# Performance work log

Measured on AMD Instinct MI355X. Metric: run time of the kernel, lower is better.

## Reference

```python
import jax, jax.numpy as jnp
import numpy as np

NUM_CLASSES = 2
CONF_THRESH = 0.05
NMS_THRESH = 0.3
NMS_TOP_K = 5000
TOP_K = 750
VAR0, VAR1 = 0.1, 0.2
NEG = -1e9  # sentinel for suppressed / below-threshold scores

NUM = 16
PRIORS = 131072


def setup_inputs() -> dict:
    key = jax.random.key(0)
    k1, k2, k3 = jax.random.split(key, 3)
    loc_data = jax.random.normal(k1, (NUM, PRIORS, 4), dtype=jnp.float32)
    conf_data = jax.random.uniform(k2, (NUM * PRIORS, NUM_CLASSES), dtype=jnp.float32)
    prior_data = jax.random.uniform(k3, (PRIORS, 4), dtype=jnp.float32)
    return {"loc_data": loc_data, "conf_data": conf_data, "prior_data": prior_data}


def decode(loc, priors):
    # loc, priors: [N, 4] (cx, cy, w, h priors); SSD box decode -> (x1, y1, x2, y2)
    xy = priors[:, :2] + loc[:, :2] * VAR0 * priors[:, 2:]
    wh = priors[:, 2:] * jnp.exp(loc[:, 2:] * VAR1)
    return jnp.concatenate([xy - wh * 0.5, xy + wh * 0.5], axis=-1)


def _area(b):
    return (b[..., 2] - b[..., 0]) * (b[..., 3] - b[..., 1])


def iou_one_to_many(box, boxes):
    # box: [4], boxes: [K, 4]
    lt = jnp.maximum(box[:2], boxes[:, :2])
    rb = jnp.minimum(box[2:], boxes[:, 2:])
    wh = jnp.clip(rb - lt, 0.0)
    inter = wh[:, 0] * wh[:, 1]
    union = _area(box) + _area(boxes) - inter
    return inter / jnp.maximum(union, 1e-12)


def nms_single(boxes, scores):
    # boxes: [P, 4], scores: [P] (one image, one class) -> [TOP_K, 5] (score, x1, y1, x2, y2)
    s = jnp.where(scores > CONF_THRESH, scores, NEG)
    top_s, top_i = jax.lax.top_k(s, NMS_TOP_K)
    top_b = boxes[top_i]  # [K, 4]
    idx_range = jnp.arange(NMS_TOP_K)

    def step(s_work, _):
        idx = jnp.argmax(s_work)
        sc = s_work[idx]
        valid = sc > NEG * 0.5
        box = top_b[idx]
        ious = iou_one_to_many(box, top_b)
        kill = (ious > NMS_THRESH) | (idx_range == idx)
        s_new = jnp.where(kill, NEG, s_work)
        row = jnp.where(valid, jnp.concatenate([sc[None], box]), jnp.zeros((5,), boxes.dtype))
        return s_new, row

    _, rows = jax.lax.scan(step, top_s, None, length=TOP_K)
    return rows  # [TOP_K, 5]


def reference(loc_data, conf_data, prior_data):
    num, P, _ = loc_data.shape
    conf = conf_data.reshape(num, P, NUM_CLASSES).transpose(0, 2, 1)  # [num, C, P]
    batch_priors = jnp.broadcast_to(prior_data, (num, P, 4)).reshape(-1, 4)
    boxes = decode(loc_data.reshape(-1, 4), batch_priors).reshape(num, P, 4)
    # NMS over non-background classes, vmapped over batch and class
    per_image = jax.vmap(nms_single, in_axes=(None, 0))          # over classes
    det = jax.vmap(per_image)(boxes, conf[:, 1:, :])             # [num, C-1, TOP_K, 5]
    bg = jnp.zeros((num, 1, TOP_K, 5), det.dtype)
    return jnp.concatenate([bg, det], axis=1)                     # [num, C, TOP_K, 5]
```

## Files before the change

### kernel.cpp

```cpp
#include <hip/hip_runtime.h>
#include <cmath>

#pragma clang fp contract(off)

typedef unsigned long long ull;

#define NPRIORS 131072
#define NIMG 16
#define KSEL 5000
#define TOPK 750
#define SORTN 8192
#define MW 80
#define NCHUNK 79
#define KSELP (NCHUNK * 64)
#define NBIN 65536
#define NSLOT 16

#define MID03 0.30000002682209014892578125

#define WS_PAIRS 0
#define WS_NDIAG 0
#define WS_MCNT 1048576
#define WS_BOXES 1048832
#define WS_SCORES 2328832
#define WS_MASK 2649088
#define WS_HIST (WS_MASK)
#define WS_CNT  (WS_MASK + 4194304)
#define WS_POS  (WS_MASK + 8388608)
#define WS_DIAG (WS_MASK + (size_t)NIMG * KSEL * MW * 8)

__device__ inline ull readlane64(ull t, int l) {
  unsigned lo = (unsigned)__builtin_amdgcn_readlane((int)(unsigned)t, l);
  unsigned hi = (unsigned)__builtin_amdgcn_readlane((int)(unsigned)(t >> 32), l);
  return ((ull)hi << 32) | lo;
}

__global__ __launch_bounds__(256) void hist_kernel(const float* __restrict__ conf,
                                                   unsigned int* __restrict__ hist) {
  const int img = blockIdx.y;
  const float4* c4 = (const float4*)conf + (size_t)img * (NPRIORS / 2);
  unsigned int* H = hist + (size_t)img * NBIN;
  for (int q = blockIdx.x * 256 + threadIdx.x; q < NPRIORS / 2; q += 64 * 256) {
    float4 v = c4[q];
    if (v.y > 0.05f) atomicAdd(&H[(__float_as_uint(v.y) >> 12) & 0xFFFFu], 1u);
    if (v.w > 0.05f) atomicAdd(&H[(__float_as_uint(v.w) >> 12) & 0xFFFFu], 1u);
  }
}

__global__ __launch_bounds__(1024) void cutoff_kernel(const unsigned int* __restrict__ hist,
                                                      unsigned int* __restrict__ pos,
                                                      int* __restrict__ meta,
                                                      float4* __restrict__ sboxes,
                                                      float* __restrict__ sscores) {
  const int img = blockIdx.x;
  const int tid = threadIdx.x;
  const int lane = tid & 63;
  const int wv = tid >> 6;
  const unsigned int* H = hist + (size_t)img * NBIN;
  unsigned int* P = pos + (size_t)img * NBIN;
  __shared__ unsigned int csum[1024];
  __shared__ unsigned int suf[1024];
  __shared__ int s_cc;
  __shared__ unsigned int s_cut, s_mc;

  for (int g = 0; g < 64; ++g) {
    unsigned int v = H[g * 1024 + tid];
    for (int m = 1; m < 64; m <<= 1) v += __shfl_xor(v, m);
    if (lane == 0) csum[g * 16 + wv] = v;
  }
  __syncthreads();
  suf[tid] = csum[tid];
  if (tid == 0) s_cc = 0;
  __syncthreads();
  for (int off = 1; off < 1024; off <<= 1) {
    unsigned int v = (tid + off < 1024) ? suf[tid + off] : 0u;
    __syncthreads();
    suf[tid] += v;
    __syncthreads();
  }
  if (suf[tid] >= KSEL && (suf[tid] - csum[tid]) < KSEL) s_cc = tid;
  __syncthreads();
  const int cc = s_cc;
  if (tid == 0) { s_cut = (unsigned int)(cc * 64); s_mc = suf[0]; }
  __syncthreads();
  for (int b = cc * 64 + tid; b < NBIN; b += 1024) {
    int q = b >> 6;
    unsigned int acc = (q + 1 < 1024) ? suf[q + 1] : 0u;
    for (int b2 = b + 1; b2 < (q + 1) * 64; ++b2) acc += H[b2];
    P[b] = acc;
    unsigned int h = H[b];
    if (acc < KSEL && acc + h >= KSEL) { s_cut = (unsigned int)b; s_mc = acc + h; }
  }
  __syncthreads();
  if (tid == 0) {
    meta[img] = (int)min(s_mc, (unsigned int)SORTN);
    meta[16 + img] = (int)s_cut;
  }
  for (int i = tid; i < KSEL; i += 1024) {
    sboxes[(size_t)img * KSEL + i] = make_float4(0.f, 0.f, 0.f, 0.f);
    sscores[(size_t)img * KSEL + i] = -1e9f;
  }
}

__global__ __launch_bounds__(256) void scatter_kernel(const float* __restrict__ conf,
                                                      const unsigned int* __restrict__ pos,
                                                      unsigned int* __restrict__ cnt,
                                                      const int* __restrict__ meta,
                                                      ull* __restrict__ pairs) {
  const int img = blockIdx.y;
  const float4* c4 = (const float4*)conf + (size_t)img * (NPRIORS / 2);
  const unsigned int* P = pos + (size_t)img * NBIN;
  unsigned int* Cn = cnt + (size_t)img * NBIN;
  ull* mypairs = pairs + (size_t)img * SORTN;
  const unsigned int cutval = ((unsigned int)meta[16 + img]) << 12;
  for (int q = blockIdx.x * 256 + threadIdx.x; q < NPRIORS / 2; q += 64 * 256) {
    float4 v = c4[q];
#pragma unroll
    for (int h = 0; h < 2; ++h) {
      float sc = h ? v.w : v.y;
      unsigned int p = 2 * (unsigned int)q + h;
      if (sc > 0.05f) {
        unsigned int u = __float_as_uint(sc);
        if (u >= cutval) {
          unsigned int bin = (u >> 12) & 0xFFFFu;
          unsigned int slot = atomicAdd(&Cn[bin], 1u);
          unsigned int idx = P[bin] + slot;
          if (idx < SORTN)
            mypairs[idx] = ((ull)u << 32) | (ull)(0xFFFFFFFFu - p);
        }
      }
    }
  }
}

__global__ __launch_bounds__(256) void rank_decode_kernel(const ull* __restrict__ pairs,
                                                          const unsigned int* __restrict__ hist,
                                                          const unsigned int* __restrict__ pos,
                                                          const int* __restrict__ meta,
                                                          const float* __restrict__ loc,
                                                          const float* __restrict__ prior,
                                                          float4* __restrict__ sboxes,
                                                          float* __restrict__ sscores) {
#pragma clang fp contract(off)
  const int img = blockIdx.y;
  const int s = blockIdx.x * 256 + threadIdx.x;
  const int mc = meta[img];
  if (s >= mc) return;
  const ull* mypairs = pairs + (size_t)img * SORTN;
  const ull key = mypairs[s];
  const unsigned int u = (unsigned int)(key >> 32);
  const unsigned int bin = (u >> 12) & 0xFFFFu;
  const unsigned int base = pos[(size_t)img * NBIN + bin];
  const unsigned int cb = hist[(size_t)img * NBIN + bin];
  const int end = min((int)(base + cb), mc);
  int rank = 0;
  for (int j = (int)base; j < end; ++j) rank += (mypairs[j] > key);
  const int fp = (int)base + rank;
  if (fp >= KSEL) return;
  const unsigned int p = 0xFFFFFFFFu - (unsigned int)(key & 0xFFFFFFFFu);
  const float* lp = loc + ((size_t)img * NPRIORS + p) * 4;
  const float* pp = prior + (size_t)p * 4;
  float l0 = lp[0], l1 = lp[1], l2 = lp[2], l3 = lp[3];
  float px = pp[0], py = pp[1], pw = pp[2], ph = pp[3];
  float cx = px + (l0 * 0.1f) * pw;
  float cy = py + (l1 * 0.1f) * ph;
  float w = pw * (float)exp((double)(l2 * 0.2f));
  float hh = ph * (float)exp((double)(l3 * 0.2f));
  float4 box;
  box.x = cx - w * 0.5f;
  box.y = cy - hh * 0.5f;
  box.z = cx + w * 0.5f;
  box.w = cy + hh * 0.5f;
  sboxes[(size_t)img * KSEL + fp] = box;
  sscores[(size_t)img * KSEL + fp] = __uint_as_float(u);
}

__global__ __launch_bounds__(256) void mask_build_kernel(const float4* __restrict__ sboxes,
                                                         ull* __restrict__ mask,
                                                         ull* __restrict__ diag,
                                                         ull* __restrict__ ndiag) {
#pragma clang fp contract(off)
  const int jt = blockIdx.x;
  const int sp = blockIdx.y;
  const int img = blockIdx.z;
  if (jt < (sp >> 1)) return;
  const int tid = threadIdx.x;
  const int lane = tid & 63;
  const int wave = tid >> 6;
  __shared__ float4 ib[128];
  const float4* bb = sboxes + (size_t)img * KSEL;
  if (tid < 128) {
    int i = sp * 128 + tid;
    ib[tid] = (i < KSEL) ? bb[i] : make_float4(0.f, 0.f, 0.f, 0.f);
  }
  __syncthreads();
  float4 cb[4];
  float ca[4];
#pragma unroll
  for (int s = 0; s < 4; ++s) {
    int j = jt * 256 + s * 64 + lane;
    cb[s] = (j < KSEL) ? bb[j] : make_float4(0.f, 0.f, 0.f, 0.f);
    ca[s] = (cb[s].z - cb[s].x) * (cb[s].w - cb[s].y);
  }
  ull* mrow = mask + (size_t)img * KSEL * MW;
  ull* dg = diag + (size_t)img * KSELP;
  ull* ndg = ndiag + (size_t)img * KSELP;
  const int grp0 = jt * 4;
  for (int k = 0; k < 32; ++k) {
    const int rr = wave * 32 + k;
    const int strip = 2 * sp + (rr >> 6);
    const int r = rr & 63;
    const int i = sp * 128 + rr;
    const float4 pb = ib[rr];
    const float pa = (pb.z - pb.x) * (pb.w - pb.y);
    ull w[4];
#pragma unroll
    for (int s = 0; s < 4; ++s) {
      float ltx = fmaxf(pb.x, cb[s].x), lty = fmaxf(pb.y, cb[s].y);
      float rbx = fminf(pb.z, cb[s].z), rby = fminf(pb.w, cb[s].w);
      float ww = fmaxf(rbx - ltx, 0.0f), hh = fmaxf(rby - lty, 0.0f);
      float inter = ww * hh;
      float uni = fmaxf(pa + ca[s] - inter, 1e-12f);
      bool cond = ((grp0 + s) != strip) | (lane > r);
      bool kill = cond && ((double)inter > MID03 * (double)uni);
      w[s] = __ballot(kill);
    }
    if (lane == 0 && i < KSEL) {
      ull* wp = mrow + (size_t)i * MW + grp0;
      ((ulonglong2*)wp)[0] = make_ulonglong2(w[0], w[1]);
      ((ulonglong2*)wp)[1] = make_ulonglong2(w[2], w[3]);
#pragma unroll
      for (int s = 0; s < 4; ++s) {
        if (grp0 + s == strip) dg[i] = w[s];
        if (grp0 + s == strip + 1) ndg[i] = w[s];
      }
    }
  }
}

__global__ __launch_bounds__(64) void sweep_kernel(const ull* __restrict__ mask,
                                                   const ull* __restrict__ diag,
                                                   const ull* __restrict__ ndiag,
                                                   const float4* __restrict__ sboxes,
                                                   const float* __restrict__ sscores,
                                                   const int* __restrict__ meta,
                                                   float* __restrict__ out) {
  const int img = blockIdx.x;
  const int lane = threadIdx.x;
  const int V = min(meta[img], KSEL);
  const ull* mb = mask + (size_t)img * KSEL * MW;
  const ull* dg = diag + (size_t)img * KSELP;
  const ull* ng = ndiag + (size_t)img * KSELP;
  __shared__ ull stage[2 * NSLOT * 128];
  __shared__ int picks[TOPK];
  __shared__ int s_n;
  const int lc = min(lane, 39);

  ull rlo = 0ULL, rhi = 0ULL;
  int nkeep = 0;

  if (V > 0) {
    int reg = 0;
    bool pendingPrev = false;
    int lastrow = 0;
    ull bridge = 0ULL;
    ull dw = dg[lane];
    ull ndw = ng[lane];
    for (int c = 0; c * 64 < V; ++c) {
      const int base = c * 64;
      const int nidx = min(base + 64 + lane, KSELP - 1);
      ull dwn = dg[nidx];
      ull ndwn = ng[nidx];
      ull t = (c & 1) ? rhi : rlo;
      ull cur = readlane64(t, c >> 1) | bridge;
      bridge = 0ULL;
      const int lim = V - base;
      ull validm = (lim >= 64) ? ~0ULL : ((~0ULL) >> (64 - lim));
      ull avail = (~cur) & validm;

      int nb = 0;
      bool full = false;
      while (avail != 0ULL) {
        int r = __builtin_ctzll(avail);
        int row = base + r;
        if (lane == 0) picks[nkeep] = row;
        lastrow = row;
        nkeep++;
        if (nkeep >= TOPK) { full = true; break; }
        __builtin_amdgcn_global_load_lds(
            (const __attribute__((address_space(1))) unsigned int*)(mb + (size_t)row * MW + 2 * lc),
            (__attribute__((address_space(3))) unsigned int*)&stage[(reg * NSLOT + nb) * 128], 16, 0, 0);
        nb++;
        ull dr = readlane64(dw, r);
        bridge |= readlane64(ndw, r);
        avail &= ~(dr | (1ULL << r));
        if (nb == NSLOT) {
          if (pendingPrev) {
            __builtin_amdgcn_s_waitcnt(0x4F70);
            asm volatile("" ::: "memory");
#pragma unroll
            for (int q = 0; q < NSLOT; ++q) {
              ulonglong2 v = *(ulonglong2*)&stage[((1 - reg) * NSLOT + q) * 128 + 2 * lane];
              rlo |= v.x; rhi |= v.y;
            }
          }
          pendingPrev = true;
          reg = 1 - reg;
          nb = 0;
        }
      }
      if (full) break;
      for (; nb < NSLOT; ++nb)
        __builtin_amdgcn_global_load_lds(
            (const __attribute__((address_space(1))) unsigned int*)(mb + (size_t)lastrow * MW + 2 * lc),
            (__attribute__((address_space(3))) unsigned int*)&stage[(reg * NSLOT + nb) * 128], 16, 0, 0);
      if (pendingPrev) {
        __builtin_amdgcn_s_waitcnt(0x4F70);
        asm volatile("" ::: "memory");
#pragma unroll
        for (int q = 0; q < NSLOT; ++q) {
          ulonglong2 v = *(ulonglong2*)&stage[((1 - reg) * NSLOT + q) * 128 + 2 * lane];
          rlo |= v.x; rhi |= v.y;
        }
      }
      pendingPrev = true;
      reg = 1 - reg;
      dw = dwn;
      ndw = ndwn;
    }
  }
  __builtin_amdgcn_s_waitcnt(0xF70);
  asm volatile("" ::: "memory");

  if (lane == 0) s_n = (nkeep < TOPK) ? nkeep : TOPK;
  __syncthreads();
  const int n = s_n;
  float* ob = out + (size_t)img * (2 * TOPK * 5) + TOPK * 5;
  for (int k = lane; k < n; k += 64) {
    int i = picks[k];
    float4 b = sboxes[(size_t)img * KSEL + i];
    float sc = sscores[(size_t)img * KSEL + i];
    float* o = ob + (size_t)k * 5;
    o[0] = sc; o[1] = b.x; o[2] = b.y; o[3] = b.z; o[4] = b.w;
  }
}

extern "C" void kernel_launch(void* const* d_in, const int* in_sizes, int n_in,
                              void* d_out, int out_size, void* d_ws, size_t ws_size,
                              hipStream_t stream) {
  const float* loc = (const float*)d_in[0];
  const float* conf = (const float*)d_in[1];
  const float* prior = (const float*)d_in[2];
  float* out = (float*)d_out;

  char* ws = (char*)d_ws;
  ull* pairs = (ull*)(ws + WS_PAIRS);
  ull* ndiag = (ull*)(ws + WS_NDIAG);
  int* meta = (int*)(ws + WS_MCNT);
  float4* sboxes = (float4*)(ws + WS_BOXES);
  float* sscores = (float*)(ws + WS_SCORES);
  ull* mask = (ull*)(ws + WS_MASK);
  ull* diag = (ull*)(ws + WS_DIAG);
  unsigned int* hist = (unsigned int*)(ws + WS_HIST);
  unsigned int* cnt = (unsigned int*)(ws + WS_CNT);
  unsigned int* pos = (unsigned int*)(ws + WS_POS);

  hipMemsetAsync(d_out, 0, (size_t)out_size * sizeof(float), stream);
  hipMemsetAsync(ws + WS_HIST, 0, 2u * 4194304u, stream);

  {
    dim3 g(64, NIMG);
    hist_kernel<<<g, 256, 0, stream>>>(conf, hist);
  }
  cutoff_kernel<<<NIMG, 1024, 0, stream>>>(hist, pos, meta, sboxes, sscores);
  {
    dim3 g(64, NIMG);
    scatter_kernel<<<g, 256, 0, stream>>>(conf, pos, cnt, meta, pairs);
  }
  {
    dim3 g((SORTN + 255) / 256, NIMG);
    rank_decode_kernel<<<g, 256, 0, stream>>>(pairs, hist, pos, meta, loc, prior, sboxes, sscores);
  }
  {
    dim3 g(20, 40, NIMG);
    mask_build_kernel<<<g, 256, 0, stream>>>(sboxes, mask, diag, ndiag);
  }
  sweep_kernel<<<NIMG, 64, 0, stream>>>(mask, diag, ndiag, sboxes, sscores, meta, out);
}
```

Measured before the change: 586.3 us.

## Split NMS sweep into producer/consumer waves with LDS mailbox handoff

The sweep kernel now uses two wavefronts per image. Wave A picks surviving rows chunk by chunk using the diagonal masks. Wave B ORs the full mask rows of the previous chunk's picks, using batched global loads into registers, and posts the next chunk's removal word to a shared mailbox. This replaces the single-wave global_load_lds double-buffer staging and is meant to overlap pick selection with mask accumulation. The cost is a block barrier per chunk and a one-chunk lag, so wave A must wait for wave B's word before every chunk.

```diff
diff --git a/kernel.cpp b/kernel.cpp
--- a/kernel.cpp
+++ b/kernel.cpp
@@ -14,7 +14,6 @@
 #define NCHUNK 79
 #define KSELP (NCHUNK * 64)
 #define NBIN 65536
-#define NSLOT 16
 
 #define MID03 0.30000002682209014892578125
 
@@ -33,6 +32,10 @@
   unsigned lo = (unsigned)__builtin_amdgcn_readlane((int)(unsigned)t, l);
   unsigned hi = (unsigned)__builtin_amdgcn_readlane((int)(unsigned)(t >> 32), l);
   return ((ull)hi << 32) | lo;
+}
+
+__device__ inline void softBarrier() {
+  asm volatile("s_waitcnt lgkmcnt(0)\n\ts_barrier" ::: "memory");
 }
 
 __global__ __launch_bounds__(256) void hist_kernel(const float* __restrict__ conf,
@@ -238,109 +241,104 @@
   }
 }
 
-__global__ __launch_bounds__(64) void sweep_kernel(const ull* __restrict__ mask,
-                                                   const ull* __restrict__ diag,
-                                                   const ull* __restrict__ ndiag,
-                                                   const float4* __restrict__ sboxes,
-                                                   const float* __restrict__ sscores,
-                                                   const int* __restrict__ meta,
-                                                   float* __restrict__ out) {
+__global__ __launch_bounds__(128) void sweep_kernel(const ull* __restrict__ mask,
+                                                    const ull* __restrict__ diag,
+                                                    const ull* __restrict__ ndiag,
+                                                    const float4* __restrict__ sboxes,
+                                                    const float* __restrict__ sscores,
+                                                    const int* __restrict__ meta,
+                                                    float* __restrict__ out) {
   const int img = blockIdx.x;
-  const int lane = threadIdx.x;
+  const int tid = threadIdx.x;
+  const int lane = tid & 63;
+  const bool waveA = (tid < 64);
   const int V = min(meta[img], KSEL);
   const ull* mb = mask + (size_t)img * KSEL * MW;
   const ull* dg = diag + (size_t)img * KSELP;
   const ull* ng = ndiag + (size_t)img * KSELP;
-  __shared__ ull stage[2 * NSLOT * 128];
-  __shared__ int picks[TOPK];
+  __shared__ ull mailbox[NCHUNK + 1];
+  __shared__ int pickbuf[TOPK];
+  __shared__ int s_np[NCHUNK];
+  __shared__ int s_start[NCHUNK];
+  __shared__ int s_done;
   __shared__ int s_n;
   const int lc = min(lane, 39);
 
-  ull rlo = 0ULL, rhi = 0ULL;
-  int nkeep = 0;
+  for (int i = tid; i <= NCHUNK; i += 128) mailbox[i] = 0ULL;
+  if (tid == 0) { s_done = 0; s_n = 0; }
+  __syncthreads();
 
   if (V > 0) {
-    int reg = 0;
-    bool pendingPrev = false;
-    int lastrow = 0;
-    ull bridge = 0ULL;
-    ull dw = dg[lane];
-    ull ndw = ng[lane];
-    for (int c = 0; c * 64 < V; ++c) {
-      const int base = c * 64;
-      const int nidx = min(base + 64 + lane, KSELP - 1);
-      ull dwn = dg[nidx];
-      ull ndwn = ng[nidx];
-      ull t = (c & 1) ? rhi : rlo;
-      ull cur = readlane64(t, c >> 1) | bridge;
-      bridge = 0ULL;
-      const int lim = V - base;
-      ull validm = (lim >= 64) ? ~0ULL : ((~0ULL) >> (64 - lim));
-      ull avail = (~cur) & validm;
-
-      int nb = 0;
-      bool full = false;
-      while (avail != 0ULL) {
-        int r = __builtin_ctzll(avail);
-        int row = base + r;
-        if (lane == 0) picks[nkeep] = row;
-        lastrow = row;
-        nkeep++;
-        if (nkeep >= TOPK) { full = true; break; }
-        __builtin_amdgcn_global_load_lds(
-            (const __attribute__((address_space(1))) unsigned int*)(mb + (size_t)row * MW + 2 * lc),
-            (__attribute__((address_space(3))) unsigned int*)&stage[(reg * NSLOT + nb) * 128], 16, 0, 0);
-        nb++;
-        ull dr = readlane64(dw, r);
-        bridge |= readlane64(ndw, r);
-        avail &= ~(dr | (1ULL << r));
-        if (nb == NSLOT) {
-          if (pendingPrev) {
-            __builtin_amdgcn_s_waitcnt(0x4F70);
-            asm volatile("" ::: "memory");
-#pragma unroll
-            for (int q = 0; q < NSLOT; ++q) {
-              ulonglong2 v = *(ulonglong2*)&stage[((1 - reg) * NSLOT + q) * 128 + 2 * lane];
-              rlo |= v.x; rhi |= v.y;
-            }
+    ull dw = 0, ndw = 0, bridge = 0;
+    ull rlo = 0, rhi = 0;
+    int nkeep = 0;
+    bool adone = false;
+    if (waveA) { dw = dg[lane]; ndw = ng[lane]; }
+
+    for (int k = 0; k < NCHUNK; ++k) {
+      softBarrier();
+      if (s_done) break;
+      if (waveA) {
+        if (!adone) {
+          const int base = k * 64;
+          const int nidx = min(base + 64 + lane, KSELP - 1);
+          ull dwn = dg[nidx];
+          ull ndwn = ng[nidx];
+          ull cur = mailbox[k] | bridge;
+          bridge = 0ULL;
+          const int lim = V - base;
+          ull validm = (lim >= 64) ? ~0ULL : ((~0ULL) >> (64 - lim));
+          ull avail = (~cur) & validm;
+          const int st = nkeep;
+          if (lane == 0) s_start[k] = st;
+          while (avail != 0ULL && nkeep < TOPK) {
+            int r = __builtin_ctzll(avail);
+            if (lane == 0) pickbuf[nkeep] = base + r;
+            nkeep++;
+            ull dr = readlane64(dw, r);
+            bridge |= readlane64(ndw, r);
+            avail &= ~(dr | (1ULL << r));
           }
-          pendingPrev = true;
-          reg = 1 - reg;
-          nb = 0;
+          if (lane == 0) s_np[k] = nkeep - st;
+          if (nkeep >= TOPK || base + 64 >= V) {
+            if (lane == 0) { s_done = 1; s_n = (nkeep < TOPK) ? nkeep : TOPK; }
+            adone = true;
+          }
+          dw = dwn;
+          ndw = ndwn;
+        }
+      } else if (k >= 1) {
+        const int np = s_np[k - 1];
+        const int st = s_start[k - 1];
+        for (int g = 0; g < np; g += 16) {
+          ulonglong2 v[16];
+#pragma unroll
+          for (int q = 0; q < 16; ++q) {
+            int t = min(g + q, np - 1);
+            int row = pickbuf[st + t];
+            v[q] = *(const ulonglong2*)(mb + (size_t)row * MW + 2 * lc);
+          }
+#pragma unroll
+          for (int q = 0; q < 16; ++q) { rlo |= v[q].x; rhi |= v[q].y; }
+        }
+        const int w = k + 1;
+        if (w < NCHUNK) {
+          ull t = (w & 1) ? rhi : rlo;
+          ull word = readlane64(t, w >> 1);
+          if (lane == 0) mailbox[w] = word;
         }
       }
-      if (full) break;
-      for (; nb < NSLOT; ++nb)
-        __builtin_amdgcn_global_load_lds(
-            (const __attribute__((address_space(1))) unsigned int*)(mb + (size_t)lastrow * MW + 2 * lc),
-            (__attribute__((address_space(3))) unsigned int*)&stage[(reg * NSLOT + nb) * 128], 16, 0, 0);
-      if (pendingPrev) {
-        __builtin_amdgcn_s_waitcnt(0x4F70);
-        asm volatile("" ::: "memory");
-#pragma unroll
-        for (int q = 0; q < NSLOT; ++q) {
-          ulonglong2 v = *(ulonglong2*)&stage[((1 - reg) * NSLOT + q) * 128 + 2 * lane];
-          rlo |= v.x; rhi |= v.y;
-        }
-      }
-      pendingPrev = true;
-      reg = 1 - reg;
-      dw = dwn;
-      ndw = ndwn;
     }
   }
-  __builtin_amdgcn_s_waitcnt(0xF70);
-  asm volatile("" ::: "memory");
-
-  if (lane == 0) s_n = (nkeep < TOPK) ? nkeep : TOPK;
+
   __syncthreads();
   const int n = s_n;
   float* ob = out + (size_t)img * (2 * TOPK * 5) + TOPK * 5;
-  for (int k = lane; k < n; k += 64) {
-    int i = picks[k];
+  for (int j = tid; j < n; j += 128) {
+    int i = pickbuf[j];
     float4 b = sboxes[(size_t)img * KSEL + i];
     float sc = sscores[(size_t)img * KSEL + i];
-    float* o = ob + (size_t)k * 5;
+    float* o = ob + (size_t)j * 5;
     o[0] = sc; o[1] = b.x; o[2] = b.y; o[3] = b.z; o[4] = b.w;
   }
 }
@@ -385,5 +383,5 @@
     dim3 g(20, 40, NIMG);
     mask_build_kernel<<<g, 256, 0, stream>>>(sboxes, mask, diag, ndiag);
   }
-  sweep_kernel<<<NIMG, 64, 0, stream>>>(mask, diag, ndiag, sboxes, sscores, meta, out);
-}
+  sweep_kernel<<<NIMG, 128, 0, stream>>>(mask, diag, ndiag, sboxes, sscores, meta, out);
+}
```

After: 534.4 us. 8.9% less time.
